# Kernel optimization log

Measured on AMD Instinct MI355X. Metric: run time of the kernel, lower is better.

## Reference

```python
import jax, jax.numpy as jnp
import numpy as np

NUM_NODES = 100000
EMB_DIM = 64
NUM_LAYERS = 3
NUM_EDGES = 3200000
NUM_QUERY = 1000000


def setup_inputs() -> dict:
    key = jax.random.key(0)
    k1, k2, k3 = jax.random.split(key, 3)
    # Xavier-uniform embedding table (learned parameter)
    limit = float(np.sqrt(6.0 / (NUM_NODES + EMB_DIM)))
    emb = jax.random.uniform(k1, (NUM_NODES, EMB_DIM), jnp.float32, -limit, limit)
    edge_index = jax.random.randint(k2, (2, NUM_EDGES), 0, NUM_NODES, dtype=jnp.int64)
    edge_label_index = jax.random.randint(k3, (2, NUM_QUERY), 0, NUM_NODES, dtype=jnp.int64)
    return {"emb": emb, "edge_index": edge_index, "edge_label_index": edge_label_index}


def reference(emb, edge_index, edge_label_index):
    src, dst = edge_index[0], edge_index[1]
    # gcn_norm without self-loops (LGConv default): deg over destination nodes
    deg = jax.ops.segment_sum(jnp.ones_like(src, dtype=emb.dtype), dst,
                              num_segments=NUM_NODES)
    dis = jnp.where(deg > 0, jax.lax.rsqrt(jnp.maximum(deg, 1.0)), 0.0)
    norm = (dis[src] * dis[dst])[:, None]  # [E,1]

    alpha = 1.0 / (NUM_LAYERS + 1)
    x = emb
    out = x * alpha
    for _ in range(NUM_LAYERS):
        # SpMM: out[dst] += norm * x[src]
        x = jax.ops.segment_sum(x[src] * norm, dst, num_segments=NUM_NODES)
        out = out + x * alpha

    # dot-product scoring of query pairs
    return jnp.sum(out[edge_label_index[0]] * out[edge_label_index[1]], axis=-1)
```

## Files before the change

kernel.cpp:

```cpp
#include <hip/hip_runtime.h>
#include <hip/hip_fp16.h>

#define NUM_NODES 100000
#define EMB_DIM   64
#define NUM_LAYERS 3
#define NUM_EDGES 3200000
#define NUM_QUERY 1000000

#define BSHIFT   6
#define BNODES   64
#define NBUCKETS ((NUM_NODES + BNODES - 1) / BNODES)
#define SRC_MASK 131071
#define NCHUNK   128
#define CHUNK    (NUM_EDGES / NCHUNK)

__global__ __launch_bounds__(256) void chist_kernel(const int* __restrict__ dst,
                                                    int* __restrict__ hist_g) {
    __shared__ int h[NBUCKETS];
    int b = blockIdx.x, tid = threadIdx.x;
    for (int k = tid; k < NBUCKETS; k += 256) h[k] = 0;
    __syncthreads();
    int beg = b * CHUNK, end = beg + CHUNK;
    for (int i = beg + tid; i < end; i += 256)
        atomicAdd(&h[dst[i] >> BSHIFT], 1);
    __syncthreads();
    for (int k = tid; k < NBUCKETS; k += 256)
        hist_g[b * NBUCKETS + k] = h[k];
}

__global__ void bscan_kernel(int* __restrict__ hist_g, int* __restrict__ bcnt) {
    int gw   = (blockIdx.x * blockDim.x + threadIdx.x) >> 6;
    int lane = threadIdx.x & 63;
    if (gw >= NBUCKETS) return;
    int c0 = 2 * lane, c1 = 2 * lane + 1;
    int v0 = hist_g[c0 * NBUCKETS + gw];
    int v1 = hist_g[c1 * NBUCKETS + gw];
    int pair = v0 + v1, x = pair;
    #pragma unroll
    for (int d = 1; d < 64; d <<= 1) {
        int y = __shfl_up(x, d);
        if (lane >= d) x += y;
    }
    int ex = x - pair;
    hist_g[c0 * NBUCKETS + gw] = ex;
    hist_g[c1 * NBUCKETS + gw] = ex + v0;
    if (lane == 63) bcnt[gw] = x;
}

__global__ void scan_kernel(const int* __restrict__ bcnt, int* __restrict__ boffs) {
    __shared__ int tile[1024];
    __shared__ int carry;
    int t = threadIdx.x;
    if (t == 0) { carry = 0; boffs[0] = 0; }
    __syncthreads();
    for (int base = 0; base < NBUCKETS; base += 1024) {
        int v = (base + t < NBUCKETS) ? bcnt[base + t] : 0;
        tile[t] = v;
        __syncthreads();
        for (int d = 1; d < 1024; d <<= 1) {
            int add = (t >= d) ? tile[t - d] : 0;
            __syncthreads();
            tile[t] += add;
            __syncthreads();
        }
        int inc = tile[t] + carry;
        if (base + t < NBUCKETS) boffs[base + t + 1] = inc;
        __syncthreads();
        if (t == 1023) carry = inc;
        __syncthreads();
    }
}

__global__ __launch_bounds__(256) void cscatter_kernel(
        const int* __restrict__ src, const int* __restrict__ dst,
        const int* __restrict__ boffs, const int* __restrict__ hist_g,
        int* __restrict__ packed) {
    __shared__ int cur[NBUCKETS];
    int b = blockIdx.x, tid = threadIdx.x;
    for (int k = tid; k < NBUCKETS; k += 256)
        cur[k] = boffs[k] + hist_g[b * NBUCKETS + k];
    __syncthreads();
    int beg = b * CHUNK, end = beg + CHUNK;
    for (int i = beg + tid; i < end; i += 256) {
        int s = src[i], d = dst[i];
        int pos = atomicAdd(&cur[d >> BSHIFT], 1);
        packed[pos] = s | ((d & 63) << 17);
    }
}

__global__ __launch_bounds__(256) void lsort_kernel(
        const int* __restrict__ boffs, const int* __restrict__ packed,
        int* __restrict__ offs, int* __restrict__ src_srt, float* __restrict__ dis) {
    __shared__ int cnt[BNODES];
    int b   = blockIdx.x;
    int tid = threadIdx.x;
    int beg = boffs[b];
    int end = boffs[b + 1];
    if (tid < BNODES) cnt[tid] = 0;
    __syncthreads();
    for (int i = beg + tid; i < end; i += 256)
        atomicAdd(&cnt[(packed[i] >> 17) & 63], 1);
    __syncthreads();
    if (tid < 64) {
        int v = cnt[tid];
        int x = v;
        #pragma unroll
        for (int d = 1; d < 64; d <<= 1) {
            int y = __shfl_up(x, d);
            if (tid >= d) x += y;
        }
        int ex = x - v;
        int node = (b << BSHIFT) + tid;
        if (node <= NUM_NODES) offs[node] = beg + ex;
        if (node <  NUM_NODES) dis[node] = (v > 0) ? rsqrtf((float)v) : 0.0f;
        cnt[tid] = ex;
    }
    __syncthreads();
    for (int i = beg + tid; i < end; i += 256) {
        int p  = packed[i];
        int pos = beg + atomicAdd(&cnt[(p >> 17) & 63], 1);
        src_srt[pos] = p & SRC_MASK;
    }
}

__global__ void prescale_kernel(const float4* __restrict__ emb4, const float* __restrict__ dis,
                                __half2* __restrict__ y2) {
    int i = blockIdx.x * blockDim.x + threadIdx.x;
    int stride = gridDim.x * blockDim.x;
    const int n4 = NUM_NODES * EMB_DIM / 4;
    for (; i < n4; i += stride) {
        float d = dis[i >> 4];
        float4 v = emb4[i];
        y2[2 * i]     = __floats2half2_rn(v.x * d, v.y * d);
        y2[2 * i + 1] = __floats2half2_rn(v.z * d, v.w * d);
    }
}

__global__ __launch_bounds__(256) void prop_kernel(
        const int* __restrict__ offs, const int* __restrict__ src_s,
        const float* __restrict__ dis, const __half2* __restrict__ yin2,
        __half2* __restrict__ yout2, const float2* __restrict__ emb2,
        __half2* __restrict__ outw2, float alpha, int mode) {
    int wid  = (blockIdx.x * blockDim.x + threadIdx.x) >> 6;
    int lane = threadIdx.x & 63;
    if (wid >= NUM_NODES) return;
    int sub = lane & 31;
    int par = lane >> 5;
    int beg = offs[wid];
    int end = offs[wid + 1];
    float ax = 0.0f, ay = 0.0f;
    int j = beg;
    for (; j + 8 <= end; j += 8) {
        int s0 = src_s[j + 0 + par];
        int s1 = src_s[j + 2 + par];
        int s2 = src_s[j + 4 + par];
        int s3 = src_s[j + 6 + par];
        __half2 h0 = yin2[(s0 << 5) + sub];
        __half2 h1 = yin2[(s1 << 5) + sub];
        __half2 h2 = yin2[(s2 << 5) + sub];
        __half2 h3 = yin2[(s3 << 5) + sub];
        float2 f0 = __half22float2(h0);
        float2 f1 = __half22float2(h1);
        float2 f2 = __half22float2(h2);
        float2 f3 = __half22float2(h3);
        ax += (f0.x + f1.x) + (f2.x + f3.x);
        ay += (f0.y + f1.y) + (f2.y + f3.y);
    }
    for (; j + 2 <= end; j += 2) {
        int s = src_s[j + par];
        float2 f = __half22float2(yin2[(s << 5) + sub]);
        ax += f.x; ay += f.y;
    }
    if (j < end && par == 0) {
        int s = src_s[j];
        float2 f = __half22float2(yin2[(s << 5) + sub]);
        ax += f.x; ay += f.y;
    }
    ax += __shfl_xor(ax, 32);
    ay += __shfl_xor(ay, 32);

    float dn = dis[wid];
    float xx = dn * ax, xy = dn * ay;
    int o2 = (wid << 5) + sub;
    if (mode == 0) {
        if (par == 0) {
            yout2[o2] = __floats2half2_rn(dn * xx, dn * xy);
        } else {
            float2 e = emb2[o2];
            outw2[o2] = __floats2half2_rn(alpha * (e.x + xx), alpha * (e.y + xy));
        }
    } else if (mode == 1) {
        if (par == 0) {
            yout2[o2] = __floats2half2_rn(dn * xx, dn * xy);
        } else {
            float2 w = __half22float2(outw2[o2]);
            outw2[o2] = __floats2half2_rn(fmaf(alpha, xx, w.x), fmaf(alpha, xy, w.y));
        }
    } else {
        if (par == 1) {
            float2 w = __half22float2(outw2[o2]);
            outw2[o2] = __floats2half2_rn(fmaf(alpha, xx, w.x), fmaf(alpha, xy, w.y));
        }
    }
}

#if defined(__has_builtin)
#if __has_builtin(__builtin_amdgcn_fdot2)
#define HAVE_FDOT2 1
#endif
#endif

#ifdef HAVE_FDOT2
typedef _Float16 hv2 __attribute__((ext_vector_type(2)));
__device__ __forceinline__ float dot2acc(unsigned a, unsigned b, float c) {
    hv2 ha, hb;
    __builtin_memcpy(&ha, &a, 4);
    __builtin_memcpy(&hb, &b, 4);
    return __builtin_amdgcn_fdot2(ha, hb, c, false);
}
#else
__device__ __forceinline__ float dot2acc(unsigned a, unsigned b, float c) {
    float2 fa = __half22float2(*(const __half2*)&a);
    float2 fb = __half22float2(*(const __half2*)&b);
    return fmaf(fa.y, fb.y, fmaf(fa.x, fb.x, c));
}
#endif

__global__ __launch_bounds__(256) void score_kernel(
        const int* __restrict__ qa, const int* __restrict__ qb,
        const uint4* __restrict__ x4, float* __restrict__ res) {
    int wave = (blockIdx.x * blockDim.x + threadIdx.x) >> 6;
    int lane = threadIdx.x & 63;
    int g = lane >> 2;
    int k = lane & 3;
    int q = (wave << 4) + g;
    int a = qa[q];
    int b = qb[q];
    const uint4* pa = x4 + (a << 3);
    const uint4* pb = x4 + (b << 3);
    uint4 ua0 = pa[k];     uint4 ub0 = pb[k];
    uint4 ua1 = pa[4 + k]; uint4 ub1 = pb[4 + k];
    float p = 0.0f;
    p = dot2acc(ua0.x, ub0.x, p);
    p = dot2acc(ua0.y, ub0.y, p);
    p = dot2acc(ua0.z, ub0.z, p);
    p = dot2acc(ua0.w, ub0.w, p);
    p = dot2acc(ua1.x, ub1.x, p);
    p = dot2acc(ua1.y, ub1.y, p);
    p = dot2acc(ua1.z, ub1.z, p);
    p = dot2acc(ua1.w, ub1.w, p);
    p += __shfl_xor(p, 1);
    p += __shfl_xor(p, 2);
    if (k == 0) res[q] = p;
}

extern "C" void kernel_launch(void* const* d_in, const int* in_sizes, int n_in,
                              void* d_out, int out_size, void* d_ws, size_t ws_size,
                              hipStream_t stream) {
    const float* emb  = (const float*)d_in[0];
    const int*   edge = (const int*)d_in[1];
    const int*   qidx = (const int*)d_in[2];
    float*       out  = (float*)d_out;

    const int* e_src = edge;
    const int* e_dst = edge + NUM_EDGES;
    const int* q_a   = qidx;
    const int* q_b   = qidx + NUM_QUERY;

    const size_t HBYTES = (size_t)NUM_NODES * EMB_DIM * sizeof(__half);
    char* ws = (char*)d_ws;
    size_t off = 0;
    auto carve = [&](size_t bytes) { void* p = ws + off; off += (bytes + 255) & ~(size_t)255; return p; };
    int*    hist_g  = (int*)   carve((size_t)NCHUNK * NBUCKETS * 4);
    int*    bcnt    = (int*)   carve((size_t)NBUCKETS * 4);
    int*    boffs   = (int*)   carve((size_t)(NBUCKETS + 1) * 4);
    int*    offs    = (int*)   carve((size_t)(NUM_NODES + 1) * 4);
    float*  dis     = (float*) carve((size_t)NUM_NODES * 4);
    int*    packed  = (int*)   carve((size_t)NUM_EDGES * 4);
    int*    src_srt = (int*)   carve((size_t)NUM_EDGES * 4);
    __half* yA      = (__half*)carve(HBYTES);
    __half* yB      = (__half*)carve(HBYTES);
    __half* outw    = (__half*)carve(HBYTES);

    const float alpha = 1.0f / (NUM_LAYERS + 1);

    chist_kernel<<<NCHUNK, 256, 0, stream>>>(e_dst, hist_g);
    bscan_kernel<<<(NBUCKETS * 64 + 255) / 256, 256, 0, stream>>>(hist_g, bcnt);
    scan_kernel<<<1, 1024, 0, stream>>>(bcnt, boffs);
    cscatter_kernel<<<NCHUNK, 256, 0, stream>>>(e_src, e_dst, boffs, hist_g, packed);
    lsort_kernel<<<NBUCKETS, 256, 0, stream>>>(boffs, packed, offs, src_srt, dis);
    prescale_kernel<<<2048, 256, 0, stream>>>((const float4*)emb, dis, (__half2*)yA);

    const int PROP_BLOCKS = (NUM_NODES * 64 + 255) / 256;
    prop_kernel<<<PROP_BLOCKS, 256, 0, stream>>>(offs, src_srt, dis,
        (const __half2*)yA, (__half2*)yB, (const float2*)emb, (__half2*)outw, alpha, 0);
    prop_kernel<<<PROP_BLOCKS, 256, 0, stream>>>(offs, src_srt, dis,
        (const __half2*)yB, (__half2*)yA, (const float2*)emb, (__half2*)outw, alpha, 1);
    prop_kernel<<<PROP_BLOCKS, 256, 0, stream>>>(offs, src_srt, dis,
        (const __half2*)yA, (__half2*)yB, (const float2*)emb, (__half2*)outw, alpha, 2);

    score_kernel<<<NUM_QUERY / 64, 256, 0, stream>>>(q_a, q_b, (const uint4*)outw, out);
}
```

Before: 364.1 us.

## Widen CSR build parallelism, vectorize edge reads, unroll SpMM gather deeper

Doubles the number of edge chunks in histogram/scatter and further splits each scatter block into two bucket halves, so twice as many blocks run (each half rescans its chunk but only writes its own buckets). Edge indices are read as int4, and the block-prefix scan now handles four chunks per lane. The propagation kernel makes row bounds wave-uniform with readfirstlane and gathers 8 neighbor rows per half-wave per iteration instead of 4, adding memory-level parallelism. The scatter change doubles edge reads and adds branch divergence in exchange for occupancy.

Result: faster. 299.6 us, median of 2 (-17.7%).

```diff
diff --git a/kernel.cpp b/kernel.cpp
--- a/kernel.cpp
+++ b/kernel.cpp
@@ -10,19 +10,26 @@
 #define BSHIFT   6
 #define BNODES   64
 #define NBUCKETS ((NUM_NODES + BNODES - 1) / BNODES)
+#define HALF1    782
 #define SRC_MASK 131071
-#define NCHUNK   128
+#define NCHUNK   256
 #define CHUNK    (NUM_EDGES / NCHUNK)
-
-__global__ __launch_bounds__(256) void chist_kernel(const int* __restrict__ dst,
+#define CHUNK4   (CHUNK / 4)
+
+__global__ __launch_bounds__(256) void chist_kernel(const int* __restrict__ keys,
                                                     int* __restrict__ hist_g) {
     __shared__ int h[NBUCKETS];
     int b = blockIdx.x, tid = threadIdx.x;
     for (int k = tid; k < NBUCKETS; k += 256) h[k] = 0;
     __syncthreads();
-    int beg = b * CHUNK, end = beg + CHUNK;
-    for (int i = beg + tid; i < end; i += 256)
-        atomicAdd(&h[dst[i] >> BSHIFT], 1);
+    const int4* k4 = (const int4*)(keys + b * CHUNK);
+    for (int i = tid; i < CHUNK4; i += 256) {
+        int4 d = k4[i];
+        atomicAdd(&h[d.x >> BSHIFT], 1);
+        atomicAdd(&h[d.y >> BSHIFT], 1);
+        atomicAdd(&h[d.z >> BSHIFT], 1);
+        atomicAdd(&h[d.w >> BSHIFT], 1);
+    }
     __syncthreads();
     for (int k = tid; k < NBUCKETS; k += 256)
         hist_g[b * NBUCKETS + k] = h[k];
@@ -32,18 +39,21 @@
     int gw   = (blockIdx.x * blockDim.x + threadIdx.x) >> 6;
     int lane = threadIdx.x & 63;
     if (gw >= NBUCKETS) return;
-    int c0 = 2 * lane, c1 = 2 * lane + 1;
-    int v0 = hist_g[c0 * NBUCKETS + gw];
-    int v1 = hist_g[c1 * NBUCKETS + gw];
-    int pair = v0 + v1, x = pair;
+    int v0 = hist_g[(4 * lane + 0) * NBUCKETS + gw];
+    int v1 = hist_g[(4 * lane + 1) * NBUCKETS + gw];
+    int v2 = hist_g[(4 * lane + 2) * NBUCKETS + gw];
+    int v3 = hist_g[(4 * lane + 3) * NBUCKETS + gw];
+    int quad = v0 + v1 + v2 + v3, x = quad;
     #pragma unroll
     for (int d = 1; d < 64; d <<= 1) {
         int y = __shfl_up(x, d);
         if (lane >= d) x += y;
     }
-    int ex = x - pair;
-    hist_g[c0 * NBUCKETS + gw] = ex;
-    hist_g[c1 * NBUCKETS + gw] = ex + v0;
+    int ex = x - quad;
+    hist_g[(4 * lane + 0) * NBUCKETS + gw] = ex;
+    hist_g[(4 * lane + 1) * NBUCKETS + gw] = ex + v0;
+    hist_g[(4 * lane + 2) * NBUCKETS + gw] = ex + v0 + v1;
+    hist_g[(4 * lane + 3) * NBUCKETS + gw] = ex + v0 + v1 + v2;
     if (lane == 63) bcnt[gw] = x;
 }
 
@@ -76,15 +86,27 @@
         const int* __restrict__ boffs, const int* __restrict__ hist_g,
         int* __restrict__ packed) {
     __shared__ int cur[NBUCKETS];
-    int b = blockIdx.x, tid = threadIdx.x;
+    int b = blockIdx.x >> 1, half = blockIdx.x & 1;
+    int LO = half ? HALF1 : 0;
+    int HI = half ? NBUCKETS : HALF1;
+    int tid = threadIdx.x;
     for (int k = tid; k < NBUCKETS; k += 256)
         cur[k] = boffs[k] + hist_g[b * NBUCKETS + k];
     __syncthreads();
-    int beg = b * CHUNK, end = beg + CHUNK;
-    for (int i = beg + tid; i < end; i += 256) {
-        int s = src[i], d = dst[i];
-        int pos = atomicAdd(&cur[d >> BSHIFT], 1);
-        packed[pos] = s | ((d & 63) << 17);
+    const int4* s4 = (const int4*)(src + b * CHUNK);
+    const int4* d4 = (const int4*)(dst + b * CHUNK);
+    for (int i = tid; i < CHUNK4; i += 256) {
+        int4 s = s4[i];
+        int4 d = d4[i];
+        int bk;
+        bk = d.x >> BSHIFT;
+        if (bk >= LO && bk < HI) { int p = atomicAdd(&cur[bk], 1); packed[p] = s.x | ((d.x & 63) << 17); }
+        bk = d.y >> BSHIFT;
+        if (bk >= LO && bk < HI) { int p = atomicAdd(&cur[bk], 1); packed[p] = s.y | ((d.y & 63) << 17); }
+        bk = d.z >> BSHIFT;
+        if (bk >= LO && bk < HI) { int p = atomicAdd(&cur[bk], 1); packed[p] = s.z | ((d.z & 63) << 17); }
+        bk = d.w >> BSHIFT;
+        if (bk >= LO && bk < HI) { int p = atomicAdd(&cur[bk], 1); packed[p] = s.w | ((d.w & 63) << 17); }
     }
 }
 
@@ -146,15 +168,55 @@
     if (wid >= NUM_NODES) return;
     int sub = lane & 31;
     int par = lane >> 5;
-    int beg = offs[wid];
-    int end = offs[wid + 1];
+    int beg = __builtin_amdgcn_readfirstlane(offs[wid]);
+    int end = __builtin_amdgcn_readfirstlane(offs[wid + 1]);
     float ax = 0.0f, ay = 0.0f;
     int j = beg;
-    for (; j + 8 <= end; j += 8) {
-        int s0 = src_s[j + 0 + par];
-        int s1 = src_s[j + 2 + par];
-        int s2 = src_s[j + 4 + par];
-        int s3 = src_s[j + 6 + par];
+    for (; j + 16 <= end; j += 16) {
+        int i0  = src_s[j + 0],  i1  = src_s[j + 1];
+        int i2  = src_s[j + 2],  i3  = src_s[j + 3];
+        int i4  = src_s[j + 4],  i5  = src_s[j + 5];
+        int i6  = src_s[j + 6],  i7  = src_s[j + 7];
+        int i8  = src_s[j + 8],  i9  = src_s[j + 9];
+        int i10 = src_s[j + 10], i11 = src_s[j + 11];
+        int i12 = src_s[j + 12], i13 = src_s[j + 13];
+        int i14 = src_s[j + 14], i15 = src_s[j + 15];
+        int s0 = par ? i1  : i0;
+        int s1 = par ? i3  : i2;
+        int s2 = par ? i5  : i4;
+        int s3 = par ? i7  : i6;
+        int s4 = par ? i9  : i8;
+        int s5 = par ? i11 : i10;
+        int s6 = par ? i13 : i12;
+        int s7 = par ? i15 : i14;
+        __half2 h0 = yin2[(s0 << 5) + sub];
+        __half2 h1 = yin2[(s1 << 5) + sub];
+        __half2 h2 = yin2[(s2 << 5) + sub];
+        __half2 h3 = yin2[(s3 << 5) + sub];
+        __half2 h4 = yin2[(s4 << 5) + sub];
+        __half2 h5 = yin2[(s5 << 5) + sub];
+        __half2 h6 = yin2[(s6 << 5) + sub];
+        __half2 h7 = yin2[(s7 << 5) + sub];
+        float2 f0 = __half22float2(h0);
+        float2 f1 = __half22float2(h1);
+        float2 f2 = __half22float2(h2);
+        float2 f3 = __half22float2(h3);
+        float2 f4 = __half22float2(h4);
+        float2 f5 = __half22float2(h5);
+        float2 f6 = __half22float2(h6);
+        float2 f7 = __half22float2(h7);
+        ax += ((f0.x + f1.x) + (f2.x + f3.x)) + ((f4.x + f5.x) + (f6.x + f7.x));
+        ay += ((f0.y + f1.y) + (f2.y + f3.y)) + ((f4.y + f5.y) + (f6.y + f7.y));
+    }
+    if (j + 8 <= end) {
+        int i0 = src_s[j + 0], i1 = src_s[j + 1];
+        int i2 = src_s[j + 2], i3 = src_s[j + 3];
+        int i4 = src_s[j + 4], i5 = src_s[j + 5];
+        int i6 = src_s[j + 6], i7 = src_s[j + 7];
+        int s0 = par ? i1 : i0;
+        int s1 = par ? i3 : i2;
+        int s2 = par ? i5 : i4;
+        int s3 = par ? i7 : i6;
         __half2 h0 = yin2[(s0 << 5) + sub];
         __half2 h1 = yin2[(s1 << 5) + sub];
         __half2 h2 = yin2[(s2 << 5) + sub];
@@ -165,6 +227,7 @@
         float2 f3 = __half22float2(h3);
         ax += (f0.x + f1.x) + (f2.x + f3.x);
         ay += (f0.y + f1.y) + (f2.y + f3.y);
+        j += 8;
     }
     for (; j + 2 <= end; j += 2) {
         int s = src_s[j + par];
@@ -287,7 +350,7 @@
     chist_kernel<<<NCHUNK, 256, 0, stream>>>(e_dst, hist_g);
     bscan_kernel<<<(NBUCKETS * 64 + 255) / 256, 256, 0, stream>>>(hist_g, bcnt);
     scan_kernel<<<1, 1024, 0, stream>>>(bcnt, boffs);
-    cscatter_kernel<<<NCHUNK, 256, 0, stream>>>(e_src, e_dst, boffs, hist_g, packed);
+    cscatter_kernel<<<NCHUNK * 2, 256, 0, stream>>>(e_src, e_dst, boffs, hist_g, packed);
     lsort_kernel<<<NBUCKETS, 256, 0, stream>>>(boffs, packed, offs, src_srt, dis);
     prescale_kernel<<<2048, 256, 0, stream>>>((const float4*)emb, dis, (__half2*)yA);
 
```
